# Performance work log

Hardware: AMD Instinct MI355X
Metric: run time of the kernel (lower is better)

## Reference

```python
import jax, jax.numpy as jnp
import numpy as np

B, S, D, H = 4, 2048, 512, 8
HD = D // H  # head_dim = 64


def setup_inputs() -> dict:
    key = jax.random.key(0)
    ks = jax.random.split(key, 6)
    s = 1.0 / np.sqrt(D)
    return {
        "value": jax.random.normal(ks[0], (B, S, D), jnp.float32),
        "key": jax.random.normal(ks[1], (B, S, D), jnp.float32),
        "query": jax.random.normal(ks[2], (B, S, D), jnp.float32),
        "Wv": jax.random.normal(ks[3], (D, D), jnp.float32) * s,
        "bv": jnp.zeros((D,), jnp.float32),
        "Wk": jax.random.normal(ks[4], (D, D), jnp.float32) * s,
        "bk": jnp.zeros((D,), jnp.float32),
        "Wq": jax.random.normal(ks[5], (D, D), jnp.float32) * s,
        "bq": jnp.zeros((D,), jnp.float32),
    }


def _heads(x):
    # [B,S,D] -> [B,H,S,hd]
    return x.reshape(B, S, H, HD).transpose(0, 2, 1, 3)


def reference(value, key, query, Wv, bv, Wk, bk, Wq, bq):
    v = _heads(value @ Wv.T + bv)
    k = _heads(key @ Wk.T + bk)
    q = _heads(query @ Wq.T + bq)
    scale = 1.0 / jnp.sqrt(jnp.asarray(HD, q.dtype))
    # two scaled-dot-product score maps, each [B,H,S,S]
    att_kq = jax.nn.softmax(jnp.einsum("bhqd,bhkd->bhqk", q, k) * scale, axis=-1)
    att_vq = jax.nn.softmax(jnp.einsum("bhqd,bhkd->bhqk", q, v) * scale, axis=-1)
    att_map = att_kq + att_vq
    fused = v + k  # [B,H,S,hd]
    attended = jnp.einsum("bhqk,bhkd->bhqd", att_map, fused)
    # elementwise multiply with q, reduce over the sequence (query) axis
    head_logits = jnp.sum(attended * q, axis=2)  # [B,H,hd]
    return head_logits.reshape(B, H * HD)
```

## Files before the change

kernel.cpp:

```cpp
#include <hip/hip_runtime.h>
#include <hip/hip_bf16.h>

#define Bq 4
#define Sq 2048
#define Dq 512
#define Hq 8
#define HDq 64

typedef __attribute__((ext_vector_type(8))) short short8;
typedef __attribute__((ext_vector_type(4))) float f32x4;

#if __has_builtin(__builtin_amdgcn_exp2f)
#define EXP2(x) __builtin_amdgcn_exp2f(x)
#else
#define EXP2(x) exp2f(x)
#endif

#define SCALE2 (0.125f * 1.44269504088896340736f)
#define INV_SCALE2 (5.545177444479562f)

__device__ __forceinline__ short bfs(float x) {
    __hip_bfloat16 h = __float2bfloat16(x);
    short r;
    __builtin_memcpy(&r, &h, 2);
    return r;
}

__device__ __forceinline__ short8 cvt8(float4 a, float4 b) {
    union { __hip_bfloat16 h[8]; short8 s; } u;
    u.h[0] = __float2bfloat16(a.x); u.h[1] = __float2bfloat16(a.y);
    u.h[2] = __float2bfloat16(a.z); u.h[3] = __float2bfloat16(a.w);
    u.h[4] = __float2bfloat16(b.x); u.h[5] = __float2bfloat16(b.y);
    u.h[6] = __float2bfloat16(b.z); u.h[7] = __float2bfloat16(b.w);
    return u.s;
}

__device__ __forceinline__ void gload16(const void* g, void* l) {
    __builtin_amdgcn_global_load_lds(
        (const __attribute__((address_space(1))) unsigned int*)g,
        (__attribute__((address_space(3))) unsigned int*)l, 16, 0, 0);
}

__global__ __launch_bounds__(256, 3)
void proj_kernel(const float* __restrict__ Xv, const float* __restrict__ Xk, const float* __restrict__ Xq,
                 const float* __restrict__ Wv, const float* __restrict__ Wk, const float* __restrict__ Wq,
                 const float* __restrict__ bv, const float* __restrict__ bk, const float* __restrict__ bq,
                 __hip_bfloat16* __restrict__ Ov, __hip_bfloat16* __restrict__ Ok, __hip_bfloat16* __restrict__ Oq) {
    __shared__ alignas(16) short As[128 * 64];
    __shared__ alignas(16) short Bs[128 * 64];

    const int z = blockIdx.z;
    const float* X   = (z == 0) ? Xv : (z == 1) ? Xk : Xq;
    const float* W   = (z == 0) ? Wv : (z == 1) ? Wk : Wq;
    const float* bia = (z == 0) ? bv : (z == 1) ? bk : bq;
    __hip_bfloat16* O = (z == 0) ? Ov : (z == 1) ? Ok : Oq;
    const float sc = (z == 2) ? SCALE2 : 1.0f;

    const int tid  = threadIdx.x;
    const int lane = tid & 63;
    const int w    = tid >> 6;
    const int wr   = w >> 1;
    const int wc   = w & 1;
    const int m0   = blockIdx.y * 128;
    const int n0   = blockIdx.x * 128;
    const int arow = lane & 15;
    const int ag   = lane >> 4;

    f32x4 acc[4][4];
    #pragma unroll
    for (int t = 0; t < 4; ++t)
        #pragma unroll
        for (int u = 0; u < 4; ++u) acc[t][u] = (f32x4){0.f, 0.f, 0.f, 0.f};

    for (int kk = 0; kk < Dq / 64; ++kk) {
        __syncthreads();
        #pragma unroll
        for (int p = 0; p < 4; ++p) {
            int id  = p * 256 + tid;
            int row = id >> 3;
            int c   = id & 7;
            int dst = row * 128 + ((c * 16) ^ ((row & 7) << 4));
            const float* ax = X + (size_t)(m0 + row) * Dq + kk * 64 + c * 8;
            const float* bx = W + (size_t)(n0 + row) * Dq + kk * 64 + c * 8;
            float4 a0 = *(const float4*)ax;
            float4 a1 = *(const float4*)(ax + 4);
            float4 b0 = *(const float4*)bx;
            float4 b1 = *(const float4*)(bx + 4);
            *(short8*)((char*)As + dst) = cvt8(a0, a1);
            *(short8*)((char*)Bs + dst) = cvt8(b0, b1);
        }
        __syncthreads();
        #pragma unroll
        for (int h = 0; h < 2; ++h) {
            short8 af[4], bf[4];
            #pragma unroll
            for (int t = 0; t < 4; ++t) {
                int ra = wr * 64 + t * 16 + arow;
                int rb = wc * 64 + t * 16 + arow;
                af[t] = *(const short8*)((const char*)As + ra * 128 + ((h * 64 + ag * 16) ^ ((ra & 7) << 4)));
                bf[t] = *(const short8*)((const char*)Bs + rb * 128 + ((h * 64 + ag * 16) ^ ((rb & 7) << 4)));
            }
            #pragma unroll
            for (int t = 0; t < 4; ++t)
                #pragma unroll
                for (int u = 0; u < 4; ++u)
                    acc[t][u] = __builtin_amdgcn_mfma_f32_16x16x32_bf16(af[t], bf[u], acc[t][u], 0, 0, 0);
        }
    }

    float biasv[4];
    #pragma unroll
    for (int u = 0; u < 4; ++u) biasv[u] = bia[n0 + wc * 64 + u * 16 + arow];

    #pragma unroll
    for (int t = 0; t < 4; ++t) {
        #pragma unroll
        for (int u = 0; u < 4; ++u) {
            #pragma unroll
            for (int r = 0; r < 4; ++r) {
                int m = m0 + wr * 64 + t * 16 + 4 * ag + r;
                int n = n0 + wc * 64 + u * 16 + arow;
                int b = m >> 11, s = m & 2047;
                int hh = n >> 6, hd = n & 63;
                O[((((size_t)b * Hq + hh) * Sq + s) << 6) + hd] =
                    __float2bfloat16((acc[t][u][r] + biasv[u]) * sc);
            }
        }
    }
}

__global__ __launch_bounds__(256)
void fuse_t_kernel(const __hip_bfloat16* __restrict__ Kh, const __hip_bfloat16* __restrict__ Vh,
                   __hip_bfloat16* __restrict__ Ft) {
    __shared__ float T[64][65];
    const int bh = blockIdx.x >> 5;
    const int st = blockIdx.x & 31;
    const int tid = threadIdx.x;

    #pragma unroll
    for (int p = 0; p < 2; ++p) {
        int idx = p * 256 + tid;
        int r = idx >> 3;
        int c = (idx & 7) * 8;
        size_t g = ((size_t)bh * Sq + st * 64 + r) * 64 + c;
        float4 k4 = *(const float4*)((const char*)Kh + g * 2);
        float4 v4 = *(const float4*)((const char*)Vh + g * 2);
        const __hip_bfloat16* kp = (const __hip_bfloat16*)&k4;
        const __hip_bfloat16* vp = (const __hip_bfloat16*)&v4;
        #pragma unroll
        for (int j = 0; j < 8; ++j)
            T[r][c + j] = __bfloat162float(kp[j]) + __bfloat162float(vp[j]);
    }
    __syncthreads();
    #pragma unroll
    for (int pp = 0; pp < 2; ++pp) {
        int idx = pp * 256 + tid;
        int d  = idx >> 3;
        int p8 = (idx & 7) * 8;
        alignas(16) __hip_bfloat16 tmp[8];
        #pragma unroll
        for (int j2 = 0; j2 < 8; ++j2) {
            int p = p8 + j2;
            int h  = p >> 5;
            int ag = (p >> 3) & 3;
            int j  = p & 7;
            int k  = 16 * (2 * (j >> 2) + h) + 4 * ag + (j & 3);
            tmp[j2] = __float2bfloat16(T[k][d]);
        }
        *(float4*)((char*)Ft + (((size_t)bh * 64 + d) * Sq + st * 64 + p8) * 2) = *(const float4*)tmp;
    }
}

__global__ __launch_bounds__(256, 4)
void attn_kernel(const __hip_bfloat16* __restrict__ Qh, const __hip_bfloat16* __restrict__ Kh,
                 const __hip_bfloat16* __restrict__ Vh, const __hip_bfloat16* __restrict__ Ft,
                 float* __restrict__ part) {
    __shared__ alignas(16) short Qs[64 * 64];
    __shared__ alignas(16) short Ks[64 * 64];
    __shared__ alignas(16) short Vs[64 * 64];
    __shared__ alignas(16) short Fs[64 * 64];

    const int tid  = threadIdx.x;
    const int lane = tid & 63;
    const int w    = tid >> 6;
    const int lb   = (blockIdx.x & 7) * 128 + (blockIdx.x >> 3);
    const int bh   = lb >> 5;
    const int s0   = (lb & 31) * 64;

    const char* Qbh = (const char*)(Qh + (size_t)bh * Sq * 64);
    const char* Kbh = (const char*)(Kh + (size_t)bh * Sq * 64);
    const char* Vbh = (const char*)(Vh + (size_t)bh * Sq * 64);
    const char* Fbh = (const char*)(Ft + (size_t)bh * 64 * Sq);

    #pragma unroll
    for (int p = 0; p < 2; ++p) {
        int idx = p * 256 + tid;
        int r = idx >> 3;
        int c = idx & 7;
        int swz = (r & 7) << 4;
        float4 q4 = *(const float4*)(Qbh + ((size_t)(s0 + r) * 64 + c * 8) * 2);
        *(float4*)((char*)Qs + r * 128 + ((c * 16) ^ swz)) = q4;
    }
    __syncthreads();

    const int arow = lane & 15;
    const int ag   = lane >> 4;
    const int aswz = (arow & 7) << 4;

    const int qrow = w * 16 + arow;
    short8 qa0 = *(const short8*)((const char*)Qs + qrow * 128 + ((16 * ag) ^ aswz));
    short8 qa1 = *(const short8*)((const char*)Qs + qrow * 128 + ((64 + 16 * ag) ^ aswz));

    f32x4 acc_k[4], acc_v[4];
    #pragma unroll
    for (int t = 0; t < 4; ++t) {
        acc_k[t] = (f32x4){0.f, 0.f, 0.f, 0.f};
        acc_v[t] = (f32x4){0.f, 0.f, 0.f, 0.f};
    }
    float lp_k = 0.f, lp_v = 0.f;

    int srow[2], sbyte[2];
    size_t kof[2], fof[2];
    #pragma unroll
    for (int p = 0; p < 2; ++p) {
        srow[p] = p * 32 + w * 8 + (lane >> 3);
        int scs = (lane & 7) ^ (srow[p] & 7);
        sbyte[p] = p * 4096 + w * 1024;
        kof[p] = ((size_t)srow[p] * 64 + scs * 8) * 2;
        fof[p] = ((size_t)srow[p] * Sq + scs * 8) * 2;
    }

    for (int ck = 0; ck < Sq / 64; ++ck) {
        const size_t kv0 = (size_t)ck * 64;
        __syncthreads();
        #pragma unroll
        for (int p = 0; p < 2; ++p) {
            gload16(Kbh + kv0 * 128 + kof[p], (char*)Ks + sbyte[p]);
            gload16(Vbh + kv0 * 128 + kof[p], (char*)Vs + sbyte[p]);
            gload16(Fbh + fof[p] + kv0 * 2,   (char*)Fs + sbyte[p]);
        }
        __syncthreads();

        f32x4 sk[4], sv[4];
        #pragma unroll
        for (int t = 0; t < 4; ++t) {
            sk[t] = (f32x4){0.f, 0.f, 0.f, 0.f};
            sv[t] = (f32x4){0.f, 0.f, 0.f, 0.f};
        }
        #pragma unroll
        for (int t = 0; t < 4; ++t) {
            int brow = t * 16 + arow;
            int bswz = (brow & 7) << 4;
            short8 kb0 = *(const short8*)((const char*)Ks + brow * 128 + ((16 * ag) ^ bswz));
            short8 kb1 = *(const short8*)((const char*)Ks + brow * 128 + ((64 + 16 * ag) ^ bswz));
            short8 vb0 = *(const short8*)((const char*)Vs + brow * 128 + ((16 * ag) ^ bswz));
            short8 vb1 = *(const short8*)((const char*)Vs + brow * 128 + ((64 + 16 * ag) ^ bswz));
            sk[t] = __builtin_amdgcn_mfma_f32_16x16x32_bf16(kb0, qa0, sk[t], 0, 0, 0);
            sk[t] = __builtin_amdgcn_mfma_f32_16x16x32_bf16(kb1, qa1, sk[t], 0, 0, 0);
            sv[t] = __builtin_amdgcn_mfma_f32_16x16x32_bf16(vb0, qa0, sv[t], 0, 0, 0);
            sv[t] = __builtin_amdgcn_mfma_f32_16x16x32_bf16(vb1, qa1, sv[t], 0, 0, 0);
        }

        short8 bpk[2], bpv[2];
        #pragma unroll
        for (int t = 0; t < 4; ++t) {
            #pragma unroll
            for (int r = 0; r < 4; ++r) {
                float ek = EXP2(sk[t][r]);
                float ev = EXP2(sv[t][r]);
                lp_k += ek; lp_v += ev;
                bpk[t & 1][4 * (t >> 1) + r] = bfs(ek);
                bpv[t & 1][4 * (t >> 1) + r] = bfs(ev);
            }
        }

        #pragma unroll
        for (int td = 0; td < 4; ++td) {
            int row = td * 16 + arow;
            int rswz = (row & 7) << 4;
            short8 fa0 = *(const short8*)((const char*)Fs + row * 128 + ((16 * ag) ^ rswz));
            short8 fa1 = *(const short8*)((const char*)Fs + row * 128 + ((64 + 16 * ag) ^ rswz));
            acc_k[td] = __builtin_amdgcn_mfma_f32_16x16x32_bf16(fa0, bpk[0], acc_k[td], 0, 0, 0);
            acc_k[td] = __builtin_amdgcn_mfma_f32_16x16x32_bf16(fa1, bpk[1], acc_k[td], 0, 0, 0);
            acc_v[td] = __builtin_amdgcn_mfma_f32_16x16x32_bf16(fa0, bpv[0], acc_v[td], 0, 0, 0);
            acc_v[td] = __builtin_amdgcn_mfma_f32_16x16x32_bf16(fa1, bpv[1], acc_v[td], 0, 0, 0);
        }
    }

    lp_k += __shfl_xor(lp_k, 16); lp_k += __shfl_xor(lp_k, 32);
    lp_v += __shfl_xor(lp_v, 16); lp_v += __shfl_xor(lp_v, 32);
    float ilk = INV_SCALE2 / lp_k;
    float ilv = INV_SCALE2 / lp_v;

    f32x4 c[4];
    #pragma unroll
    for (int td = 0; td < 4; ++td) {
        #pragma unroll
        for (int r = 0; r < 4; ++r) {
            int d = 16 * td + 4 * ag + r;
            int byte = 2 * d;
            float qv = __bfloat162float(*(const __hip_bfloat16*)(
                (const char*)Qs + qrow * 128 + (((byte & ~15) ^ ((qrow & 7) << 4)) | (byte & 15))));
            c[td][r] = (acc_k[td][r] * ilk + acc_v[td][r] * ilv) * qv;
        }
    }
    #pragma unroll
    for (int off = 1; off < 16; off <<= 1) {
        #pragma unroll
        for (int td = 0; td < 4; ++td) {
            #pragma unroll
            for (int r = 0; r < 4; ++r) c[td][r] += __shfl_xor(c[td][r], off);
        }
    }

    __syncthreads();
    float* part_s = (float*)Ks;
    if (arow == 0) {
        #pragma unroll
        for (int td = 0; td < 4; ++td)
            #pragma unroll
            for (int r = 0; r < 4; ++r)
                part_s[w * 64 + 16 * td + 4 * ag + r] = c[td][r];
    }
    __syncthreads();
    if (tid < 64) {
        float t = part_s[tid] + part_s[64 + tid] + part_s[128 + tid] + part_s[192 + tid];
        part[(size_t)lb * 64 + tid] = t;
    }
}

__global__ void reduce_kernel(const float* __restrict__ part, float* __restrict__ out) {
    int bh = blockIdx.x;
    int d  = threadIdx.x;
    float t = 0.f;
    for (int i = 0; i < 32; ++i)
        t += part[(size_t)(bh * 32 + i) * 64 + d];
    out[bh * 64 + d] = t;
}

extern "C" void kernel_launch(void* const* d_in, const int* in_sizes, int n_in,
                              void* d_out, int out_size, void* d_ws, size_t ws_size,
                              hipStream_t stream) {
    const float* value = (const float*)d_in[0];
    const float* key   = (const float*)d_in[1];
    const float* query = (const float*)d_in[2];
    const float* Wv    = (const float*)d_in[3];
    const float* bv    = (const float*)d_in[4];
    const float* Wk    = (const float*)d_in[5];
    const float* bk    = (const float*)d_in[6];
    const float* Wq    = (const float*)d_in[7];
    const float* bq    = (const float*)d_in[8];
    float* out = (float*)d_out;

    char* w = (char*)d_ws;
    __hip_bfloat16* Qh = (__hip_bfloat16*)(w);
    __hip_bfloat16* Kh = (__hip_bfloat16*)(w + (size_t)8  * 1024 * 1024);
    __hip_bfloat16* Vh = (__hip_bfloat16*)(w + (size_t)16 * 1024 * 1024);
    __hip_bfloat16* Ft = (__hip_bfloat16*)(w + (size_t)24 * 1024 * 1024);
    float*          part = (float*)      (w + (size_t)32 * 1024 * 1024);

    dim3 pg(Dq / 128, (Bq * Sq) / 128, 3);
    proj_kernel<<<pg, 256, 0, stream>>>(value, key, query, Wv, Wk, Wq, bv, bk, bq, Vh, Kh, Qh);

    fuse_t_kernel<<<1024, 256, 0, stream>>>(Kh, Vh, Ft);
    attn_kernel<<<1024, 256, 0, stream>>>(Qh, Kh, Vh, Ft, part);
    reduce_kernel<<<32, 64, 0, stream>>>(part, out);
}
```

Before: 132.5 us.

## Process two query tiles per wave to reuse K/V/F LDS tiles

Each block now handles 128 query rows instead of 64, with every wave computing two 16-row query tiles against the same K, V and fused tiles. This halves the number of blocks and the total global-to-LDS traffic for K, V and the fused tensor, and reuses each LDS fragment read for two MFMA tiles. The cost is doubled accumulator registers (launch bounds lowered to 2 blocks per SM), 512 blocks instead of 1024, and adjusted reduction indexing.

```diff
diff --git a/kernel.cpp b/kernel.cpp
--- a/kernel.cpp
+++ b/kernel.cpp
@@ -171,11 +171,11 @@
     }
 }
 
-__global__ __launch_bounds__(256, 4)
+__global__ __launch_bounds__(256, 2)
 void attn_kernel(const __hip_bfloat16* __restrict__ Qh, const __hip_bfloat16* __restrict__ Kh,
                  const __hip_bfloat16* __restrict__ Vh, const __hip_bfloat16* __restrict__ Ft,
                  float* __restrict__ part) {
-    __shared__ alignas(16) short Qs[64 * 64];
+    __shared__ alignas(16) short Qs[128 * 64];
     __shared__ alignas(16) short Ks[64 * 64];
     __shared__ alignas(16) short Vs[64 * 64];
     __shared__ alignas(16) short Fs[64 * 64];
@@ -183,9 +183,9 @@
     const int tid  = threadIdx.x;
     const int lane = tid & 63;
     const int w    = tid >> 6;
-    const int lb   = (blockIdx.x & 7) * 128 + (blockIdx.x >> 3);
-    const int bh   = lb >> 5;
-    const int s0   = (lb & 31) * 64;
+    const int lb   = (blockIdx.x & 7) * 64 + (blockIdx.x >> 3);
+    const int bh   = lb >> 4;
+    const int s0   = (lb & 15) * 128;
 
     const char* Qbh = (const char*)(Qh + (size_t)bh * Sq * 64);
     const char* Kbh = (const char*)(Kh + (size_t)bh * Sq * 64);
@@ -193,7 +193,7 @@
     const char* Fbh = (const char*)(Ft + (size_t)bh * 64 * Sq);
 
     #pragma unroll
-    for (int p = 0; p < 2; ++p) {
+    for (int p = 0; p < 4; ++p) {
         int idx = p * 256 + tid;
         int r = idx >> 3;
         int c = idx & 7;
@@ -207,17 +207,24 @@
     const int ag   = lane >> 4;
     const int aswz = (arow & 7) << 4;
 
-    const int qrow = w * 16 + arow;
-    short8 qa0 = *(const short8*)((const char*)Qs + qrow * 128 + ((16 * ag) ^ aswz));
-    short8 qa1 = *(const short8*)((const char*)Qs + qrow * 128 + ((64 + 16 * ag) ^ aswz));
-
-    f32x4 acc_k[4], acc_v[4];
-    #pragma unroll
-    for (int t = 0; t < 4; ++t) {
-        acc_k[t] = (f32x4){0.f, 0.f, 0.f, 0.f};
-        acc_v[t] = (f32x4){0.f, 0.f, 0.f, 0.f};
-    }
-    float lp_k = 0.f, lp_v = 0.f;
+    short8 qa[2][2];
+    #pragma unroll
+    for (int tile = 0; tile < 2; ++tile) {
+        int qr = w * 32 + tile * 16 + arow;
+        int qswz = (qr & 7) << 4;
+        qa[tile][0] = *(const short8*)((const char*)Qs + qr * 128 + ((16 * ag) ^ qswz));
+        qa[tile][1] = *(const short8*)((const char*)Qs + qr * 128 + ((64 + 16 * ag) ^ qswz));
+    }
+
+    f32x4 acc_k[2][4], acc_v[2][4];
+    #pragma unroll
+    for (int tile = 0; tile < 2; ++tile)
+        #pragma unroll
+        for (int t = 0; t < 4; ++t) {
+            acc_k[tile][t] = (f32x4){0.f, 0.f, 0.f, 0.f};
+            acc_v[tile][t] = (f32x4){0.f, 0.f, 0.f, 0.f};
+        }
+    float lp_k[2] = {0.f, 0.f}, lp_v[2] = {0.f, 0.f};
 
     int srow[2], sbyte[2];
     size_t kof[2], fof[2];
@@ -241,12 +248,14 @@
         }
         __syncthreads();
 
-        f32x4 sk[4], sv[4];
-        #pragma unroll
-        for (int t = 0; t < 4; ++t) {
-            sk[t] = (f32x4){0.f, 0.f, 0.f, 0.f};
-            sv[t] = (f32x4){0.f, 0.f, 0.f, 0.f};
-        }
+        f32x4 sk[2][4], sv[2][4];
+        #pragma unroll
+        for (int tile = 0; tile < 2; ++tile)
+            #pragma unroll
+            for (int t = 0; t < 4; ++t) {
+                sk[tile][t] = (f32x4){0.f, 0.f, 0.f, 0.f};
+                sv[tile][t] = (f32x4){0.f, 0.f, 0.f, 0.f};
+            }
         #pragma unroll
         for (int t = 0; t < 4; ++t) {
             int brow = t * 16 + arow;
@@ -255,22 +264,28 @@
             short8 kb1 = *(const short8*)((const char*)Ks + brow * 128 + ((64 + 16 * ag) ^ bswz));
             short8 vb0 = *(const short8*)((const char*)Vs + brow * 128 + ((16 * ag) ^ bswz));
             short8 vb1 = *(const short8*)((const char*)Vs + brow * 128 + ((64 + 16 * ag) ^ bswz));
-            sk[t] = __builtin_amdgcn_mfma_f32_16x16x32_bf16(kb0, qa0, sk[t], 0, 0, 0);
-            sk[t] = __builtin_amdgcn_mfma_f32_16x16x32_bf16(kb1, qa1, sk[t], 0, 0, 0);
-            sv[t] = __builtin_amdgcn_mfma_f32_16x16x32_bf16(vb0, qa0, sv[t], 0, 0, 0);
-            sv[t] = __builtin_amdgcn_mfma_f32_16x16x32_bf16(vb1, qa1, sv[t], 0, 0, 0);
-        }
-
-        short8 bpk[2], bpv[2];
-        #pragma unroll
-        for (int t = 0; t < 4; ++t) {
-            #pragma unroll
-            for (int r = 0; r < 4; ++r) {
-                float ek = EXP2(sk[t][r]);
-                float ev = EXP2(sv[t][r]);
-                lp_k += ek; lp_v += ev;
-                bpk[t & 1][4 * (t >> 1) + r] = bfs(ek);
-                bpv[t & 1][4 * (t >> 1) + r] = bfs(ev);
+            #pragma unroll
+            for (int tile = 0; tile < 2; ++tile) {
+                sk[tile][t] = __builtin_amdgcn_mfma_f32_16x16x32_bf16(kb0, qa[tile][0], sk[tile][t], 0, 0, 0);
+                sk[tile][t] = __builtin_amdgcn_mfma_f32_16x16x32_bf16(kb1, qa[tile][1], sk[tile][t], 0, 0, 0);
+                sv[tile][t] = __builtin_amdgcn_mfma_f32_16x16x32_bf16(vb0, qa[tile][0], sv[tile][t], 0, 0, 0);
+                sv[tile][t] = __builtin_amdgcn_mfma_f32_16x16x32_bf16(vb1, qa[tile][1], sv[tile][t], 0, 0, 0);
+            }
+        }
+
+        short8 bpk[2][2], bpv[2][2];
+        #pragma unroll
+        for (int tile = 0; tile < 2; ++tile) {
+            #pragma unroll
+            for (int t = 0; t < 4; ++t) {
+                #pragma unroll
+                for (int r = 0; r < 4; ++r) {
+                    float ek = EXP2(sk[tile][t][r]);
+                    float ev = EXP2(sv[tile][t][r]);
+                    lp_k[tile] += ek; lp_v[tile] += ev;
+                    bpk[tile][t & 1][4 * (t >> 1) + r] = bfs(ek);
+                    bpv[tile][t & 1][4 * (t >> 1) + r] = bfs(ev);
+                }
             }
         }
 
@@ -280,51 +295,60 @@
             int rswz = (row & 7) << 4;
             short8 fa0 = *(const short8*)((const char*)Fs + row * 128 + ((16 * ag) ^ rswz));
             short8 fa1 = *(const short8*)((const char*)Fs + row * 128 + ((64 + 16 * ag) ^ rswz));
-            acc_k[td] = __builtin_amdgcn_mfma_f32_16x16x32_bf16(fa0, bpk[0], acc_k[td], 0, 0, 0);
-            acc_k[td] = __builtin_amdgcn_mfma_f32_16x16x32_bf16(fa1, bpk[1], acc_k[td], 0, 0, 0);
-            acc_v[td] = __builtin_amdgcn_mfma_f32_16x16x32_bf16(fa0, bpv[0], acc_v[td], 0, 0, 0);
-            acc_v[td] = __builtin_amdgcn_mfma_f32_16x16x32_bf16(fa1, bpv[1], acc_v[td], 0, 0, 0);
-        }
-    }
-
-    lp_k += __shfl_xor(lp_k, 16); lp_k += __shfl_xor(lp_k, 32);
-    lp_v += __shfl_xor(lp_v, 16); lp_v += __shfl_xor(lp_v, 32);
-    float ilk = INV_SCALE2 / lp_k;
-    float ilv = INV_SCALE2 / lp_v;
-
-    f32x4 c[4];
-    #pragma unroll
-    for (int td = 0; td < 4; ++td) {
-        #pragma unroll
-        for (int r = 0; r < 4; ++r) {
-            int d = 16 * td + 4 * ag + r;
-            int byte = 2 * d;
-            float qv = __bfloat162float(*(const __hip_bfloat16*)(
-                (const char*)Qs + qrow * 128 + (((byte & ~15) ^ ((qrow & 7) << 4)) | (byte & 15))));
-            c[td][r] = (acc_k[td][r] * ilk + acc_v[td][r] * ilv) * qv;
-        }
-    }
-    #pragma unroll
-    for (int off = 1; off < 16; off <<= 1) {
-        #pragma unroll
-        for (int td = 0; td < 4; ++td) {
-            #pragma unroll
-            for (int r = 0; r < 4; ++r) c[td][r] += __shfl_xor(c[td][r], off);
+            #pragma unroll
+            for (int tile = 0; tile < 2; ++tile) {
+                acc_k[tile][td] = __builtin_amdgcn_mfma_f32_16x16x32_bf16(fa0, bpk[tile][0], acc_k[tile][td], 0, 0, 0);
+                acc_k[tile][td] = __builtin_amdgcn_mfma_f32_16x16x32_bf16(fa1, bpk[tile][1], acc_k[tile][td], 0, 0, 0);
+                acc_v[tile][td] = __builtin_amdgcn_mfma_f32_16x16x32_bf16(fa0, bpv[tile][0], acc_v[tile][td], 0, 0, 0);
+                acc_v[tile][td] = __builtin_amdgcn_mfma_f32_16x16x32_bf16(fa1, bpv[tile][1], acc_v[tile][td], 0, 0, 0);
+            }
         }
     }
 
     __syncthreads();
     float* part_s = (float*)Ks;
-    if (arow == 0) {
-        #pragma unroll
-        for (int td = 0; td < 4; ++td)
-            #pragma unroll
-            for (int r = 0; r < 4; ++r)
-                part_s[w * 64 + 16 * td + 4 * ag + r] = c[td][r];
+    #pragma unroll
+    for (int tile = 0; tile < 2; ++tile) {
+        float lk = lp_k[tile], lv = lp_v[tile];
+        lk += __shfl_xor(lk, 16); lk += __shfl_xor(lk, 32);
+        lv += __shfl_xor(lv, 16); lv += __shfl_xor(lv, 32);
+        float ilk = INV_SCALE2 / lk;
+        float ilv = INV_SCALE2 / lv;
+
+        int qr = w * 32 + tile * 16 + arow;
+        f32x4 c[4];
+        #pragma unroll
+        for (int td = 0; td < 4; ++td) {
+            #pragma unroll
+            for (int r = 0; r < 4; ++r) {
+                int d = 16 * td + 4 * ag + r;
+                int byte = 2 * d;
+                float qv = __bfloat162float(*(const __hip_bfloat16*)(
+                    (const char*)Qs + qr * 128 + (((byte & ~15) ^ ((qr & 7) << 4)) | (byte & 15))));
+                c[td][r] = (acc_k[tile][td][r] * ilk + acc_v[tile][td][r] * ilv) * qv;
+            }
+        }
+        #pragma unroll
+        for (int off = 1; off < 16; off <<= 1) {
+            #pragma unroll
+            for (int td = 0; td < 4; ++td) {
+                #pragma unroll
+                for (int r = 0; r < 4; ++r) c[td][r] += __shfl_xor(c[td][r], off);
+            }
+        }
+        if (arow == 0) {
+            #pragma unroll
+            for (int td = 0; td < 4; ++td)
+                #pragma unroll
+                for (int r = 0; r < 4; ++r)
+                    part_s[(w * 2 + tile) * 64 + 16 * td + 4 * ag + r] = c[td][r];
+        }
     }
     __syncthreads();
     if (tid < 64) {
-        float t = part_s[tid] + part_s[64 + tid] + part_s[128 + tid] + part_s[192 + tid];
+        float t = 0.f;
+        #pragma unroll
+        for (int r = 0; r < 8; ++r) t += part_s[r * 64 + tid];
         part[(size_t)lb * 64 + tid] = t;
     }
 }
@@ -333,8 +357,8 @@
     int bh = blockIdx.x;
     int d  = threadIdx.x;
     float t = 0.f;
-    for (int i = 0; i < 32; ++i)
-        t += part[(size_t)(bh * 32 + i) * 64 + d];
+    for (int i = 0; i < 16; ++i)
+        t += part[(size_t)(bh * 16 + i) * 64 + d];
     out[bh * 64 + d] = t;
 }
 
@@ -363,6 +387,6 @@
     proj_kernel<<<pg, 256, 0, stream>>>(value, key, query, Wv, Wk, Wq, bv, bk, bq, Vh, Kh, Qh);
 
     fuse_t_kernel<<<1024, 256, 0, stream>>>(Kh, Vh, Ft);
-    attn_kernel<<<1024, 256, 0, stream>>>(Qh, Kh, Vh, Ft, part);
+    attn_kernel<<<512, 256, 0, stream>>>(Qh, Kh, Vh, Ft, part);
     reduce_kernel<<<32, 64, 0, stream>>>(part, out);
 }
```

Result: faster. 121.5 us (-8.3%).
